# Kernel optimization log

Hardware: AMD Instinct MI355X
Metric: run time of the kernel (lower is better)

## Reference

```python
import jax, jax.numpy as jnp
import numpy as np

B, N, D = 8, 1024, 768
R, SH = 10, 2
H = R + SH            # 12 total heads
DH = D // H           # 64
DF = 2 * D            # FFN hidden


def _layernorm(x, g, b, eps=1e-5):
    mu = jnp.mean(x, axis=-1, keepdims=True)
    var = jnp.var(x, axis=-1, keepdims=True)
    return (x - mu) * jax.lax.rsqrt(var + eps) * g + b


def setup_inputs() -> dict:
    key = jax.random.key(0)
    ks = jax.random.split(key, 12)
    s = 0.02
    inp = {
        'nodes': jax.random.normal(ks[0], (B, N, D), dtype=jnp.float32),
        'relation_mask': jax.random.uniform(ks[1], (B, N, N, R), dtype=jnp.float32),
        'node_mask': jax.random.randint(ks[2], (B, N), 0, 2).astype(bool),
        'Wq': jax.random.normal(ks[3], (D, D), dtype=jnp.float32) * s,
        'bq': jnp.zeros((D,), jnp.float32),
        'Wk': jax.random.normal(ks[4], (D, D), dtype=jnp.float32) * s,
        'bk': jnp.zeros((D,), jnp.float32),
        'Wv': jax.random.normal(ks[5], (D, D), dtype=jnp.float32) * s,
        'bv': jnp.zeros((D,), jnp.float32),
        'Wo': jax.random.normal(ks[6], (D, D), dtype=jnp.float32) * s,
        'bo': jnp.zeros((D,), jnp.float32),
        'ln1_g': jnp.ones((D,), jnp.float32),
        'ln1_b': jnp.zeros((D,), jnp.float32),
        'W1': jax.random.normal(ks[7], (DF, D), dtype=jnp.float32) * s,
        'b1': jnp.zeros((DF,), jnp.float32),
        'W2': jax.random.normal(ks[8], (D, DF), dtype=jnp.float32) * s,
        'b2': jnp.zeros((D,), jnp.float32),
        'ln2_g': jnp.ones((D,), jnp.float32),
        'ln2_b': jnp.zeros((D,), jnp.float32),
    }
    return inp


def reference(nodes, relation_mask, node_mask, Wq, bq, Wk, bk, Wv, bv, Wo, bo,
              ln1_g, ln1_b, W1, b1, W2, b2, ln2_g, ln2_b):
    neg_inf = jnp.float32(-jnp.inf)
    # projections -> [B, H, N, DH]
    q = (nodes @ Wq.T + bq).reshape(B, N, H, DH).transpose(0, 2, 1, 3)
    k = (nodes @ Wk.T + bk).reshape(B, N, H, DH).transpose(0, 2, 1, 3)
    v = (nodes @ Wv.T + bv).reshape(B, N, H, DH).transpose(0, 2, 1, 3)
    scores = jnp.einsum('bhqd,bhkd->bhqk', q, k) / jnp.sqrt(jnp.float32(DH))
    # relation-typed gating on first R heads
    rel_gate = relation_mask.transpose(0, 3, 1, 2)          # [B, R, N, N]
    typed = jnp.where(rel_gate < 1e-4, neg_inf, scores[:, :R])
    scores = jnp.concatenate([typed, scores[:, R:]], axis=1)
    # key padding mask
    key_mask = node_mask[:, None, None, :]                  # [B,1,1,N]
    scores = jnp.where(key_mask, scores, neg_inf)
    attn = jax.nn.softmax(scores, axis=-1)
    attn = jnp.nan_to_num(attn, nan=0.0)                    # rows with no valid keys -> 0
    out = jnp.einsum('bhqk,bhkd->bhqd', attn, v)
    out = out.transpose(0, 2, 1, 3).reshape(B, N, D)
    out = out @ Wo.T + bo
    h = _layernorm(nodes + out, ln1_g, ln1_b)
    ffn = jax.nn.gelu(h @ W1.T + b1, approximate=False) @ W2.T + b2
    h = _layernorm(h + ffn, ln2_g, ln2_b)
    return h
```

## Files before the change

### kernel.cpp

```cpp
#include <hip/hip_runtime.h>
#include <stdint.h>
#include <math.h>

typedef unsigned short u16;
typedef __bf16 bf16x8 __attribute__((ext_vector_type(8)));
typedef unsigned short u16x8 __attribute__((ext_vector_type(8)));
typedef unsigned short us4 __attribute__((ext_vector_type(4)));
typedef float f32x4 __attribute__((ext_vector_type(4)));

#define DEVI __device__ __forceinline__

constexpr int B_ = 8, N_ = 1024, D_ = 768, H_ = 12, DH_ = 64, DF_ = 1536;

DEVI u16 f2bu(float f) {
  unsigned x = __builtin_bit_cast(unsigned, f);
  x += 0x7FFFu + ((x >> 16) & 1u);
  return (u16)(x >> 16);
}
DEVI float b2f(u16 u) { return __builtin_bit_cast(float, (unsigned)u << 16); }

DEVI bf16x8 ld_frag(const u16* p) {
  return __builtin_bit_cast(bf16x8, *(const u16x8*)p);
}

DEVI void gload_lds16(const u16* g, u16* l) {
  __builtin_amdgcn_global_load_lds(
      (const __attribute__((address_space(1))) void*)g,
      (__attribute__((address_space(3))) void*)l, 16, 0, 0);
}

struct CvtArgs {
  const float* src[7];
  u16* dst[7];
  int n4[7];
  int start[8];
};
__global__ __launch_bounds__(256)
void cvt_all(CvtArgs a) {
  const int gb = blockIdx.x;
  int j = 0;
  while (gb >= a.start[j + 1]) ++j;
  const int i = (gb - a.start[j]) * 256 + threadIdx.x;
  if (i >= a.n4[j]) return;
  float4 v = ((const float4*)a.src[j])[i];
  ushort4 o;
  o.x = f2bu(v.x); o.y = f2bu(v.y); o.z = f2bu(v.z); o.w = f2bu(v.w);
  ((ushort4*)a.dst[j])[i] = o;
}

__global__ __launch_bounds__(256)
void build_mask_packed(const float* __restrict__ rel, const int* __restrict__ nm,
                       u16* __restrict__ mp) {
  const int b = blockIdx.z, q0 = blockIdx.y * 16, k0 = blockIdx.x * 256;
  const int t = threadIdx.x;
  __shared__ u16 w12[16][256];
  const int key_ok = nm[(b << 10) + k0 + t];
  const float th = 1e-4f;
#pragma unroll 1
  for (int it = 0; it < 16; ++it) {
    unsigned bits;
    if (!key_ok) {
      bits = 0xFFFu;
    } else {
      const size_t idx = (((size_t)(b << 10) + q0 + it) << 10) + k0 + t;
      const float2* rp = (const float2*)(rel + idx * 10);
      float2 a0 = rp[0], a1 = rp[1], a2 = rp[2], a3 = rp[3], a4 = rp[4];
      bits  = (a0.x < th ? 1u : 0u)   | (a0.y < th ? 2u : 0u)
            | (a1.x < th ? 4u : 0u)   | (a1.y < th ? 8u : 0u)
            | (a2.x < th ? 16u : 0u)  | (a2.y < th ? 32u : 0u)
            | (a3.x < th ? 64u : 0u)  | (a3.y < th ? 128u : 0u)
            | (a4.x < th ? 256u : 0u) | (a4.y < th ? 512u : 0u);
    }
    w12[it][t ^ ((it & 7) << 1)] = (u16)bits;
  }
  __syncthreads();
  const int ql = t & 15, kt = t >> 4;
  unsigned wv[16];
#pragma unroll
  for (int j2 = 0; j2 < 8; ++j2) {
    const int e = (kt * 16 + j2 * 2) ^ ((ql & 7) << 1);
    wv[j2 * 2] = w12[ql][e];
    wv[j2 * 2 + 1] = w12[ql][e + 1];
  }
#pragma unroll
  for (int h = 0; h < 12; ++h) {
    unsigned word = 0;
#pragma unroll
    for (int j = 0; j < 16; ++j) word |= ((wv[j] >> h) & 1u) << j;
    mp[(((size_t)(b * H_ + h)) * (N_ / 16) + (k0 >> 4) + kt) * N_ + q0 + ql] = (u16)word;
  }
}

template<int EPI>
__global__ __launch_bounds__(256, 3)
void gemm_bt(const u16* __restrict__ A, const u16* __restrict__ Bm,
             const float* __restrict__ bias0, const float* __restrict__ bias1,
             const float* __restrict__ residf, const u16* __restrict__ residb,
             u16* __restrict__ out0, u16* __restrict__ out1,
             int M, int N, int K) {
  __shared__ u16 As[3][128 * 32];
  __shared__ u16 Bs[3][128 * 32];
  const int t = threadIdx.x;
  const int w = t >> 6, l = t & 63;
  const int li = l & 15, grp = l >> 4;
  const int nwg = gridDim.x * gridDim.y;
  int id = blockIdx.y * gridDim.x + blockIdx.x;
  id = (id & 7) * (nwg >> 3) + (id >> 3);
  const int by = id / gridDim.x;
  const int bx = id - by * gridDim.x;
  const int n0 = bx * 128, m0 = by * 128;
  const int wr = w >> 1, wc = w & 1;

  f32x4 acc[4][4] = {};

  const int arow = w * 16 + (l >> 2);
  const int acol = (l & 3) * 8;
  const u16* Ag = A + (size_t)(m0 + arow) * K + acol;
  const u16* Bg = Bm + (size_t)(n0 + arow) * K + acol;
  const int NT = K >> 5;

  auto stage = [&](int buf, int kt) {
    u16* Asw = &As[buf][(w * 16) * 32];
    u16* Bsw = &Bs[buf][(w * 16) * 32];
    const int k0 = kt * 32;
    gload_lds16(Ag + k0, Asw);
    gload_lds16(Ag + (size_t)64 * K + k0, Asw + 64 * 32);
    gload_lds16(Bg + k0, Bsw);
    gload_lds16(Bg + (size_t)64 * K + k0, Bsw + 64 * 32);
  };

  stage(0, 0); stage(1, 1);
  asm volatile("s_waitcnt vmcnt(4)\n\ts_barrier" ::: "memory");

  for (int kt = 0; kt < NT; ++kt) {
    const int bt = kt % 3;
    const bool pre = (kt + 2 < NT);
    if (pre) stage((kt + 2) % 3, kt + 2);
    bf16x8 af[4], bfr[4];
#pragma unroll
    for (int m = 0; m < 4; ++m)
      af[m] = ld_frag(&As[bt][(wr * 64 + m * 16 + li) * 32 + grp * 8]);
#pragma unroll
    for (int n = 0; n < 4; ++n)
      bfr[n] = ld_frag(&Bs[bt][(wc * 64 + n * 16 + li) * 32 + grp * 8]);
    __builtin_amdgcn_s_setprio(1);
#pragma unroll
    for (int m = 0; m < 4; ++m)
#pragma unroll
      for (int n = 0; n < 4; ++n)
        acc[m][n] = __builtin_amdgcn_mfma_f32_16x16x32_bf16(af[m], bfr[n], acc[m][n], 0, 0, 0);
    __builtin_amdgcn_s_setprio(0);
    if (pre) asm volatile("s_waitcnt vmcnt(4) lgkmcnt(0)\n\ts_barrier" ::: "memory");
    else     asm volatile("s_waitcnt vmcnt(0) lgkmcnt(0)\n\ts_barrier" ::: "memory");
  }

#pragma unroll
  for (int m = 0; m < 4; ++m) {
#pragma unroll
    for (int n = 0; n < 4; ++n) {
#pragma unroll
      for (int j = 0; j < 4; ++j) {
        const int row = m0 + wr * 64 + m * 16 + grp * 4 + j;
        const int col = n0 + wc * 64 + n * 16 + li;
        float v = acc[m][n][j];
        if constexpr (EPI == 0) {
          v += (col < D_) ? bias0[col] : bias1[col - D_];
          if (col < D_) v *= 0.125f;
          const int b = row >> 10, i = row & (N_ - 1);
          int c2 = (col < D_) ? col : col - D_;
          u16* dst = (col < D_) ? out0 : out1;
          dst[(((size_t)(b * H_ + (c2 >> 6))) * N_ + i) * DH_ + (c2 & 63)] = f2bu(v);
        } else if constexpr (EPI == 1) {
          v += bias0[row];
          const int b = col >> 10, i = col & (N_ - 1);
          out0[(((size_t)(b * H_ + (row >> 6))) * DH_ + (row & 63)) * N_ + i] = f2bu(v);
        } else if constexpr (EPI == 2) {
          v += bias0[col] + residf[(size_t)row * N + col];
          out0[(size_t)row * N + col] = f2bu(v);
        } else if constexpr (EPI == 3) {
          v += bias0[col];
          float gel = 0.5f * v * (1.0f + erff(v * 0.70710678118654752440f));
          out0[(size_t)row * N + col] = f2bu(gel);
        } else {
          v += bias0[col] + b2f(residb[(size_t)row * N + col]);
          out0[(size_t)row * N + col] = f2bu(v);
        }
      }
    }
  }
}

__global__ __launch_bounds__(512, 4)
void attn(const u16* __restrict__ q, const u16* __restrict__ k, const u16* __restrict__ vT,
          const u16* __restrict__ mp, u16* __restrict__ outp) {
  const int nwg = gridDim.x;
  const int p = blockIdx.x;
  const int lid = (p & 7) * (nwg >> 3) + (p >> 3);
  const int bh_i = lid >> 3;
  const int qblk = lid & 7;
  const int b = bh_i / H_, h = bh_i - (bh_i / H_) * H_;
  const int w = threadIdx.x >> 6, l = threadIdx.x & 63;
  const int li = l & 15, grp = l >> 4;
  const int qw = qblk * 128 + w * 16;
  const size_t bh = (size_t)bh_i;

  __shared__ u16 Kt[2][64 * 64];
  __shared__ u16 Vt[2][64 * 64];
  __shared__ u16 P[8][16 * 64];

  const u16* kbase = k + bh * N_ * DH_;
  const u16* vbase = vT + bh * DH_ * N_;

  const int srow_off = l >> 3;
  const int sg = l & 7;
  const int r0 = w * 8;
  auto stageK = [&](int buf, int kj0) {
    const int row = r0 + srow_off;
    const int gp = sg ^ (row & 7);
    gload_lds16(kbase + (size_t)(kj0 + row) * DH_ + gp * 8, &Kt[buf][r0 * 64]);
  };
  auto stageV = [&](int buf, int kj0) {
    const int row = r0 + srow_off;
    const int gp = sg ^ (row & 7);
    gload_lds16(vbase + (size_t)row * N_ + kj0 + gp * 8, &Vt[buf][r0 * 64]);
  };

  const u16* qp = q + (bh * N_ + qw) * DH_;
  const bf16x8 bq0 = ld_frag(qp + li * DH_ + grp * 8);
  const bf16x8 bq1 = ld_frag(qp + li * DH_ + 32 + grp * 8);

  f32x4 accO[4] = {};
  float m = -INFINITY, lsum = 0.f;

  u16* Pw = &P[w][0];
  const int sw = (li & 7) << 3;
  const int prow = li * 64;
  const u16* mrow = mp + bh * (N_ / 16) * N_ + qw + li;

  stageK(0, 0); stageV(0, 0);
  __syncthreads();
  int cur = 0;

  for (int kj0 = 0; kj0 < N_; kj0 += 64) {
    if (kj0 + 64 < N_) { stageK(cur ^ 1, kj0 + 64); stageV(cur ^ 1, kj0 + 64); }
    unsigned mword[4];
#pragma unroll
    for (int t = 0; t < 4; ++t) mword[t] = mrow[(size_t)((kj0 >> 4) + t) * N_];

    f32x4 s[4];
    __builtin_amdgcn_s_setprio(1);
#pragma unroll
    for (int t = 0; t < 4; ++t) {
      const int row = t * 16 + li;
      const int rs = row & 7;
      const bf16x8 ka0 = ld_frag(&Kt[cur][row * 64 + ((grp ^ rs) * 8)]);
      const bf16x8 ka1 = ld_frag(&Kt[cur][row * 64 + (((grp + 4) ^ rs) * 8)]);
      f32x4 z = {0.f, 0.f, 0.f, 0.f};
      z = __builtin_amdgcn_mfma_f32_16x16x32_bf16(ka0, bq0, z, 0, 0, 0);
      z = __builtin_amdgcn_mfma_f32_16x16x32_bf16(ka1, bq1, z, 0, 0, 0);
      s[t] = z;
    }
    __builtin_amdgcn_s_setprio(0);

    float sv[16];
    float rmax = -INFINITY;
#pragma unroll
    for (int t = 0; t < 4; ++t) {
      const unsigned mb = (mword[t] >> (grp * 4)) & 0xFu;
#pragma unroll
      for (int j = 0; j < 4; ++j) {
        const float x = ((mb >> j) & 1u) ? -INFINITY : s[t][j];
        sv[t * 4 + j] = x;
        rmax = fmaxf(rmax, x);
      }
    }
    rmax = fmaxf(rmax, __shfl_xor(rmax, 16));
    rmax = fmaxf(rmax, __shfl_xor(rmax, 32));
    if (!__all(rmax <= m + 8.f)) {
      const float mnew = fmaxf(m, rmax);
      const float scal = (m == -INFINITY) ? 0.f : __expf(m - mnew);
      lsum *= scal;
#pragma unroll
      for (int t2 = 0; t2 < 4; ++t2) accO[t2] *= scal;
      m = mnew;
    }
    const float msafe = (m == -INFINITY) ? 0.f : m;
    float psum = 0.f;
    float pv[16];
#pragma unroll
    for (int i = 0; i < 16; ++i) {
      const float e = __expf(sv[i] - msafe);
      pv[i] = e;
      psum += e;
    }
    psum += __shfl_xor(psum, 16);
    psum += __shfl_xor(psum, 32);
    lsum += psum;
#pragma unroll
    for (int t = 0; t < 4; ++t) {
      us4 pk;
      pk[0] = f2bu(pv[t * 4 + 0]); pk[1] = f2bu(pv[t * 4 + 1]);
      pk[2] = f2bu(pv[t * 4 + 2]); pk[3] = f2bu(pv[t * 4 + 3]);
      *(us4*)&Pw[prow + ((t * 16 + grp * 4) ^ sw)] = pk;
    }
    __builtin_amdgcn_s_setprio(1);
#pragma unroll
    for (int kc = 0; kc < 2; ++kc) {
      const bf16x8 pb = ld_frag(&Pw[prow + ((kc * 32 + grp * 8) ^ sw)]);
#pragma unroll
      for (int t2 = 0; t2 < 4; ++t2) {
        const int row = t2 * 16 + li;
        const bf16x8 va = ld_frag(&Vt[cur][row * 64 + (((kc * 4 + grp) ^ (row & 7)) * 8)]);
        accO[t2] = __builtin_amdgcn_mfma_f32_16x16x32_bf16(va, pb, accO[t2], 0, 0, 0);
      }
    }
    __builtin_amdgcn_s_setprio(0);
    __syncthreads();
    cur ^= 1;
  }
  const float inv = (lsum > 0.f) ? 1.0f / lsum : 0.f;
  u16* op = outp + ((size_t)b * N_ + qw + li) * D_ + h * DH_;
#pragma unroll
  for (int t2 = 0; t2 < 4; ++t2) {
    us4 ov;
    ov[0] = f2bu(accO[t2][0] * inv); ov[1] = f2bu(accO[t2][1] * inv);
    ov[2] = f2bu(accO[t2][2] * inv); ov[3] = f2bu(accO[t2][3] * inv);
    *(us4*)&op[t2 * 16 + grp * 4] = ov;
  }
}

template<int OUTF32>
__global__ __launch_bounds__(256)
void ln_kernel(const u16* __restrict__ x, const float* __restrict__ g,
               const float* __restrict__ be, u16* __restrict__ ybf,
               float* __restrict__ yf) {
  const int row = blockIdx.x;
  const int t = threadIdx.x;
  const u16* xr = x + (size_t)row * D_;
  const float v0 = b2f(xr[t]), v1 = b2f(xr[t + 256]), v2 = b2f(xr[t + 512]);
  float s = v0 + v1 + v2;
  float s2 = v0 * v0 + v1 * v1 + v2 * v2;
#pragma unroll
  for (int d = 1; d < 64; d <<= 1) { s += __shfl_xor(s, d); s2 += __shfl_xor(s2, d); }
  __shared__ float red[8];
  const int w = t >> 6;
  if ((t & 63) == 0) { red[w] = s; red[4 + w] = s2; }
  __syncthreads();
  s = red[0] + red[1] + red[2] + red[3];
  s2 = red[4] + red[5] + red[6] + red[7];
  const float mu = s * (1.0f / D_);
  const float var = fmaxf(s2 * (1.0f / D_) - mu * mu, 0.0f);
  const float rstd = rsqrtf(var + 1e-5f);
#pragma unroll
  for (int c = 0; c < 3; ++c) {
    const int idx = t + c * 256;
    const float vv = (c == 0) ? v0 : (c == 1) ? v1 : v2;
    const float o = (vv - mu) * rstd * g[idx] + be[idx];
    if constexpr (OUTF32) yf[(size_t)row * D_ + idx] = o;
    else ybf[(size_t)row * D_ + idx] = f2bu(o);
  }
}

extern "C" void kernel_launch(void* const* d_in, const int* in_sizes, int n_in,
                              void* d_out, int out_size, void* d_ws, size_t ws_size,
                              hipStream_t stream) {
  (void)in_sizes; (void)n_in; (void)out_size; (void)ws_size;
  const float* nodes = (const float*)d_in[0];
  const float* rel   = (const float*)d_in[1];
  const int*   nmask = (const int*)d_in[2];
  const float* Wq = (const float*)d_in[3];
  const float* bq = (const float*)d_in[4];
  const float* Wk = (const float*)d_in[5];
  const float* bk = (const float*)d_in[6];
  const float* Wv = (const float*)d_in[7];
  const float* bv = (const float*)d_in[8];
  const float* Wo = (const float*)d_in[9];
  const float* bo = (const float*)d_in[10];
  const float* ln1g = (const float*)d_in[11];
  const float* ln1b = (const float*)d_in[12];
  const float* W1 = (const float*)d_in[13];
  const float* b1 = (const float*)d_in[14];
  const float* W2 = (const float*)d_in[15];
  const float* b2 = (const float*)d_in[16];
  const float* ln2g = (const float*)d_in[17];
  const float* ln2b = (const float*)d_in[18];
  float* out = (float*)d_out;

  char* ws = (char*)d_ws;
  u16* Wqk_bf = (u16*)(ws + 0);
  u16* Wv_bf  = (u16*)(ws + 2359296);
  u16* Wo_bf  = (u16*)(ws + 3538944);
  u16* W1_bf  = (u16*)(ws + 4718592);
  u16* W2_bf  = (u16*)(ws + 7077888);
  u16* Xbf    = (u16*)(ws + 9437184);
  u16* qb     = (u16*)(ws + 22020096);
  u16* kb     = (u16*)(ws + 34603008);
  u16* vTb    = (u16*)(ws + 47185920);
  u16* mwb    = (u16*)(ws + 59768832);
  u16* prehb  = (u16*)(ws + 22020096);
  u16* hbf    = (u16*)(ws + 47185920);
  u16* f1b    = (u16*)(ws + 59768832);
  u16* preob  = (u16*)(ws + 84934656);
  u16* attno  = Xbf;

  const dim3 blk(256);
  build_mask_packed<<<dim3(4, 64, 8), blk, 0, stream>>>(rel, nmask, mwb);
  CvtArgs ca;
  ca.src[0] = Wq; ca.src[1] = Wk; ca.src[2] = Wv; ca.src[3] = Wo;
  ca.src[4] = W1; ca.src[5] = W2; ca.src[6] = nodes;
  ca.dst[0] = Wqk_bf; ca.dst[1] = Wqk_bf + 768 * 768; ca.dst[2] = Wv_bf;
  ca.dst[3] = Wo_bf; ca.dst[4] = W1_bf; ca.dst[5] = W2_bf; ca.dst[6] = Xbf;
  ca.n4[0] = ca.n4[1] = ca.n4[2] = ca.n4[3] = 147456;
  ca.n4[4] = ca.n4[5] = 294912; ca.n4[6] = 1572864;
  ca.start[0] = 0; ca.start[1] = 576; ca.start[2] = 1152; ca.start[3] = 1728;
  ca.start[4] = 2304; ca.start[5] = 3456; ca.start[6] = 4608; ca.start[7] = 10752;
  cvt_all<<<10752, blk, 0, stream>>>(ca);
  gemm_bt<0><<<dim3(12, 64), blk, 0, stream>>>(Xbf, Wqk_bf, bq, bk, nullptr, nullptr,
                                               qb, kb, 8192, 1536, 768);
  gemm_bt<1><<<dim3(64, 6), blk, 0, stream>>>(Wv_bf, Xbf, bv, nullptr, nullptr, nullptr,
                                              vTb, nullptr, 768, 8192, 768);
  attn<<<768, dim3(512), 0, stream>>>(qb, kb, vTb, mwb, attno);
  gemm_bt<2><<<dim3(6, 64), blk, 0, stream>>>(attno, Wo_bf, bo, nullptr, nodes, nullptr,
                                              prehb, nullptr, 8192, 768, 768);
  ln_kernel<0><<<8192, blk, 0, stream>>>(prehb, ln1g, ln1b, hbf, nullptr);
  gemm_bt<3><<<dim3(12, 64), blk, 0, stream>>>(hbf, W1_bf, b1, nullptr, nullptr, nullptr,
                                               f1b, nullptr, 8192, 1536, 768);
  gemm_bt<4><<<dim3(6, 64), blk, 0, stream>>>(f1b, W2_bf, b2, nullptr, nullptr, hbf,
                                              preob, nullptr, 8192, 768, 1536);
  ln_kernel<1><<<8192, blk, 0, stream>>>(preob, ln2g, ln2b, nullptr, out);
}
```

Before: 310.9 us.

## Merge mask build with conversion and fuse QK and V projection GEMMs into one launch

Folds the relation-mask packing kernel into the fp32-to-bf16 conversion kernel as extra leading blocks, and merges the Q/K projection GEMM with the transposed V projection GEMM into a single grid of 1152 tiles. This cuts two kernel launches and lets small grids share the device, which reduces tail idle time. The attention kernel also gets a tree-shaped row max and uses native bf16 conversion for packing P and the output. Risks: the mask blocks use shared memory and a barrier inside a branch, and native bf16 casts may round differently from the manual f2bu.

```diff
diff --git a/kernel.cpp b/kernel.cpp
--- a/kernel.cpp
+++ b/kernel.cpp
@@ -4,8 +4,8 @@
 
 typedef unsigned short u16;
 typedef __bf16 bf16x8 __attribute__((ext_vector_type(8)));
+typedef __bf16 bf16x2 __attribute__((ext_vector_type(2)));
 typedef unsigned short u16x8 __attribute__((ext_vector_type(8)));
-typedef unsigned short us4 __attribute__((ext_vector_type(4)));
 typedef float f32x4 __attribute__((ext_vector_type(4)));
 
 #define DEVI __device__ __forceinline__
@@ -36,78 +36,70 @@
   int start[8];
 };
 __global__ __launch_bounds__(256)
-void cvt_all(CvtArgs a) {
-  const int gb = blockIdx.x;
-  int j = 0;
-  while (gb >= a.start[j + 1]) ++j;
-  const int i = (gb - a.start[j]) * 256 + threadIdx.x;
-  if (i >= a.n4[j]) return;
-  float4 v = ((const float4*)a.src[j])[i];
-  ushort4 o;
-  o.x = f2bu(v.x); o.y = f2bu(v.y); o.z = f2bu(v.z); o.w = f2bu(v.w);
-  ((ushort4*)a.dst[j])[i] = o;
-}
-
-__global__ __launch_bounds__(256)
-void build_mask_packed(const float* __restrict__ rel, const int* __restrict__ nm,
-                       u16* __restrict__ mp) {
-  const int b = blockIdx.z, q0 = blockIdx.y * 16, k0 = blockIdx.x * 256;
+void prep_all(CvtArgs a, const float* __restrict__ rel, const int* __restrict__ nm,
+              u16* __restrict__ mp) {
+  const int gb0 = blockIdx.x;
   const int t = threadIdx.x;
-  __shared__ u16 w12[16][256];
-  const int key_ok = nm[(b << 10) + k0 + t];
-  const float th = 1e-4f;
+  if (gb0 < 2048) {
+    const int b = gb0 >> 8, q0 = ((gb0 >> 2) & 63) * 16, k0 = (gb0 & 3) * 256;
+    __shared__ u16 w12[16][256];
+    const int key_ok = nm[(b << 10) + k0 + t];
+    const float th = 1e-4f;
 #pragma unroll 1
-  for (int it = 0; it < 16; ++it) {
-    unsigned bits;
-    if (!key_ok) {
-      bits = 0xFFFu;
-    } else {
-      const size_t idx = (((size_t)(b << 10) + q0 + it) << 10) + k0 + t;
-      const float2* rp = (const float2*)(rel + idx * 10);
-      float2 a0 = rp[0], a1 = rp[1], a2 = rp[2], a3 = rp[3], a4 = rp[4];
-      bits  = (a0.x < th ? 1u : 0u)   | (a0.y < th ? 2u : 0u)
-            | (a1.x < th ? 4u : 0u)   | (a1.y < th ? 8u : 0u)
-            | (a2.x < th ? 16u : 0u)  | (a2.y < th ? 32u : 0u)
-            | (a3.x < th ? 64u : 0u)  | (a3.y < th ? 128u : 0u)
-            | (a4.x < th ? 256u : 0u) | (a4.y < th ? 512u : 0u);
-    }
-    w12[it][t ^ ((it & 7) << 1)] = (u16)bits;
-  }
-  __syncthreads();
-  const int ql = t & 15, kt = t >> 4;
-  unsigned wv[16];
-#pragma unroll
-  for (int j2 = 0; j2 < 8; ++j2) {
-    const int e = (kt * 16 + j2 * 2) ^ ((ql & 7) << 1);
-    wv[j2 * 2] = w12[ql][e];
-    wv[j2 * 2 + 1] = w12[ql][e + 1];
-  }
-#pragma unroll
-  for (int h = 0; h < 12; ++h) {
-    unsigned word = 0;
-#pragma unroll
-    for (int j = 0; j < 16; ++j) word |= ((wv[j] >> h) & 1u) << j;
-    mp[(((size_t)(b * H_ + h)) * (N_ / 16) + (k0 >> 4) + kt) * N_ + q0 + ql] = (u16)word;
+    for (int it = 0; it < 16; ++it) {
+      unsigned bits;
+      if (!key_ok) {
+        bits = 0xFFFu;
+      } else {
+        const size_t idx = (((size_t)(b << 10) + q0 + it) << 10) + k0 + t;
+        const float2* rp = (const float2*)(rel + idx * 10);
+        float2 a0 = rp[0], a1 = rp[1], a2 = rp[2], a3 = rp[3], a4 = rp[4];
+        bits  = (a0.x < th ? 1u : 0u)   | (a0.y < th ? 2u : 0u)
+              | (a1.x < th ? 4u : 0u)   | (a1.y < th ? 8u : 0u)
+              | (a2.x < th ? 16u : 0u)  | (a2.y < th ? 32u : 0u)
+              | (a3.x < th ? 64u : 0u)  | (a3.y < th ? 128u : 0u)
+              | (a4.x < th ? 256u : 0u) | (a4.y < th ? 512u : 0u);
+      }
+      w12[it][t ^ ((it & 7) << 1)] = (u16)bits;
+    }
+    __syncthreads();
+    const int ql = t & 15, kt = t >> 4;
+    unsigned wv[16];
+#pragma unroll
+    for (int j2 = 0; j2 < 8; ++j2) {
+      const int e = (kt * 16 + j2 * 2) ^ ((ql & 7) << 1);
+      wv[j2 * 2] = w12[ql][e];
+      wv[j2 * 2 + 1] = w12[ql][e + 1];
+    }
+#pragma unroll
+    for (int h = 0; h < 12; ++h) {
+      unsigned word = 0;
+#pragma unroll
+      for (int j = 0; j < 16; ++j) word |= ((wv[j] >> h) & 1u) << j;
+      mp[(((size_t)(b * H_ + h)) * (N_ / 16) + (k0 >> 4) + kt) * N_ + q0 + ql] = (u16)word;
+    }
+  } else {
+    int j = 0;
+    while (gb0 >= a.start[j + 1]) ++j;
+    const int i = (gb0 - a.start[j]) * 256 + t;
+    if (i >= a.n4[j]) return;
+    float4 v = ((const float4*)a.src[j])[i];
+    ushort4 o;
+    o.x = f2bu(v.x); o.y = f2bu(v.y); o.z = f2bu(v.z); o.w = f2bu(v.w);
+    ((ushort4*)a.dst[j])[i] = o;
   }
 }
 
 template<int EPI>
-__global__ __launch_bounds__(256, 3)
-void gemm_bt(const u16* __restrict__ A, const u16* __restrict__ Bm,
-             const float* __restrict__ bias0, const float* __restrict__ bias1,
-             const float* __restrict__ residf, const u16* __restrict__ residb,
-             u16* __restrict__ out0, u16* __restrict__ out1,
-             int M, int N, int K) {
-  __shared__ u16 As[3][128 * 32];
-  __shared__ u16 Bs[3][128 * 32];
+DEVI void gemm_body(const u16* __restrict__ A, const u16* __restrict__ Bm,
+                    const float* __restrict__ bias0, const float* __restrict__ bias1,
+                    const float* __restrict__ residf, const u16* __restrict__ residb,
+                    u16* __restrict__ out0, u16* __restrict__ out1,
+                    int N, int K, int bx, int by,
+                    u16 (&As)[3][128 * 32], u16 (&Bs)[3][128 * 32]) {
   const int t = threadIdx.x;
   const int w = t >> 6, l = t & 63;
   const int li = l & 15, grp = l >> 4;
-  const int nwg = gridDim.x * gridDim.y;
-  int id = blockIdx.y * gridDim.x + blockIdx.x;
-  id = (id & 7) * (nwg >> 3) + (id >> 3);
-  const int by = id / gridDim.x;
-  const int bx = id - by * gridDim.x;
   const int n0 = bx * 128, m0 = by * 128;
   const int wr = w >> 1, wc = w & 1;
 
@@ -190,6 +182,46 @@
   }
 }
 
+template<int EPI>
+__global__ __launch_bounds__(256, 3)
+void gemm_bt(const u16* __restrict__ A, const u16* __restrict__ Bm,
+             const float* __restrict__ bias0,
+             const float* __restrict__ residf, const u16* __restrict__ residb,
+             u16* __restrict__ out0, int N, int K) {
+  __shared__ u16 As[3][128 * 32];
+  __shared__ u16 Bs[3][128 * 32];
+  const int nwg = gridDim.x * gridDim.y;
+  int id = blockIdx.y * gridDim.x + blockIdx.x;
+  id = (id & 7) * (nwg >> 3) + (id >> 3);
+  const int by = id / gridDim.x;
+  const int bx = id - by * gridDim.x;
+  gemm_body<EPI>(A, Bm, bias0, nullptr, residf, residb, out0, nullptr,
+                 N, K, bx, by, As, Bs);
+}
+
+__global__ __launch_bounds__(256, 3)
+void gemm_qkv(const u16* __restrict__ Xbf, const u16* __restrict__ Wqk,
+              const u16* __restrict__ Wv,
+              const float* __restrict__ bq, const float* __restrict__ bk,
+              const float* __restrict__ bv,
+              u16* __restrict__ qb, u16* __restrict__ kb, u16* __restrict__ vTb) {
+  __shared__ u16 As[3][128 * 32];
+  __shared__ u16 Bs[3][128 * 32];
+  constexpr int nwg = 1152;
+  int id = blockIdx.x;
+  id = (id & 7) * (nwg >> 3) + (id >> 3);
+  if (id < 768) {
+    const int by = id / 12, bx = id - by * 12;
+    gemm_body<0>(Xbf, Wqk, bq, bk, nullptr, nullptr, qb, kb,
+                 1536, 768, bx, by, As, Bs);
+  } else {
+    const int v = id - 768;
+    const int by = v / 64, bx = v - by * 64;
+    gemm_body<1>(Wv, Xbf, bv, nullptr, nullptr, nullptr, vTb, nullptr,
+                 8192, 768, bx, by, As, Bs);
+  }
+}
+
 __global__ __launch_bounds__(512, 4)
 void attn(const u16* __restrict__ q, const u16* __restrict__ k, const u16* __restrict__ vT,
           const u16* __restrict__ mp, u16* __restrict__ outp) {
@@ -263,17 +295,19 @@
     __builtin_amdgcn_s_setprio(0);
 
     float sv[16];
-    float rmax = -INFINITY;
 #pragma unroll
     for (int t = 0; t < 4; ++t) {
       const unsigned mb = (mword[t] >> (grp * 4)) & 0xFu;
 #pragma unroll
-      for (int j = 0; j < 4; ++j) {
-        const float x = ((mb >> j) & 1u) ? -INFINITY : s[t][j];
-        sv[t * 4 + j] = x;
-        rmax = fmaxf(rmax, x);
-      }
-    }
+      for (int j = 0; j < 4; ++j)
+        sv[t * 4 + j] = ((mb >> j) & 1u) ? -INFINITY : s[t][j];
+    }
+    const float a0 = fmaxf(fmaxf(sv[0], sv[1]), sv[2]);
+    const float a1 = fmaxf(fmaxf(sv[3], sv[4]), sv[5]);
+    const float a2 = fmaxf(fmaxf(sv[6], sv[7]), sv[8]);
+    const float a3 = fmaxf(fmaxf(sv[9], sv[10]), sv[11]);
+    const float a4 = fmaxf(fmaxf(sv[12], sv[13]), sv[14]);
+    float rmax = fmaxf(fmaxf(fmaxf(a0, a1), fmaxf(a2, a3)), fmaxf(a4, sv[15]));
     rmax = fmaxf(rmax, __shfl_xor(rmax, 16));
     rmax = fmaxf(rmax, __shfl_xor(rmax, 32));
     if (!__all(rmax <= m + 8.f)) {
@@ -298,10 +332,12 @@
     lsum += psum;
 #pragma unroll
     for (int t = 0; t < 4; ++t) {
-      us4 pk;
-      pk[0] = f2bu(pv[t * 4 + 0]); pk[1] = f2bu(pv[t * 4 + 1]);
-      pk[2] = f2bu(pv[t * 4 + 2]); pk[3] = f2bu(pv[t * 4 + 3]);
-      *(us4*)&Pw[prow + ((t * 16 + grp * 4) ^ sw)] = pk;
+      bf16x2 plo = { (__bf16)pv[t * 4 + 0], (__bf16)pv[t * 4 + 1] };
+      bf16x2 phi = { (__bf16)pv[t * 4 + 2], (__bf16)pv[t * 4 + 3] };
+      uint2 pk;
+      pk.x = __builtin_bit_cast(unsigned, plo);
+      pk.y = __builtin_bit_cast(unsigned, phi);
+      *(uint2*)&Pw[prow + ((t * 16 + grp * 4) ^ sw)] = pk;
     }
     __builtin_amdgcn_s_setprio(1);
 #pragma unroll
@@ -322,10 +358,12 @@
   u16* op = outp + ((size_t)b * N_ + qw + li) * D_ + h * DH_;
 #pragma unroll
   for (int t2 = 0; t2 < 4; ++t2) {
-    us4 ov;
-    ov[0] = f2bu(accO[t2][0] * inv); ov[1] = f2bu(accO[t2][1] * inv);
-    ov[2] = f2bu(accO[t2][2] * inv); ov[3] = f2bu(accO[t2][3] * inv);
-    *(us4*)&op[t2 * 16 + grp * 4] = ov;
+    bf16x2 o01 = { (__bf16)(accO[t2][0] * inv), (__bf16)(accO[t2][1] * inv) };
+    bf16x2 o23 = { (__bf16)(accO[t2][2] * inv), (__bf16)(accO[t2][3] * inv) };
+    uint2 ov;
+    ov.x = __builtin_bit_cast(unsigned, o01);
+    ov.y = __builtin_bit_cast(unsigned, o23);
+    *(uint2*)&op[t2 * 16 + grp * 4] = ov;
   }
 }
 
@@ -404,7 +442,6 @@
   u16* attno  = Xbf;
 
   const dim3 blk(256);
-  build_mask_packed<<<dim3(4, 64, 8), blk, 0, stream>>>(rel, nmask, mwb);
   CvtArgs ca;
   ca.src[0] = Wq; ca.src[1] = Wk; ca.src[2] = Wv; ca.src[3] = Wo;
   ca.src[4] = W1; ca.src[5] = W2; ca.src[6] = nodes;
@@ -412,20 +449,17 @@
   ca.dst[3] = Wo_bf; ca.dst[4] = W1_bf; ca.dst[5] = W2_bf; ca.dst[6] = Xbf;
   ca.n4[0] = ca.n4[1] = ca.n4[2] = ca.n4[3] = 147456;
   ca.n4[4] = ca.n4[5] = 294912; ca.n4[6] = 1572864;
-  ca.start[0] = 0; ca.start[1] = 576; ca.start[2] = 1152; ca.start[3] = 1728;
-  ca.start[4] = 2304; ca.start[5] = 3456; ca.start[6] = 4608; ca.start[7] = 10752;
-  cvt_all<<<10752, blk, 0, stream>>>(ca);
-  gemm_bt<0><<<dim3(12, 64), blk, 0, stream>>>(Xbf, Wqk_bf, bq, bk, nullptr, nullptr,
-                                               qb, kb, 8192, 1536, 768);
-  gemm_bt<1><<<dim3(64, 6), blk, 0, stream>>>(Wv_bf, Xbf, bv, nullptr, nullptr, nullptr,
-                                              vTb, nullptr, 768, 8192, 768);
+  ca.start[0] = 2048; ca.start[1] = 2624; ca.start[2] = 3200; ca.start[3] = 3776;
+  ca.start[4] = 4352; ca.start[5] = 5504; ca.start[6] = 6656; ca.start[7] = 12800;
+  prep_all<<<12800, blk, 0, stream>>>(ca, rel, nmask, mwb);
+  gemm_qkv<<<1152, blk, 0, stream>>>(Xbf, Wqk_bf, Wv_bf, bq, bk, bv, qb, kb, vTb);
   attn<<<768, dim3(512), 0, stream>>>(qb, kb, vTb, mwb, attno);
-  gemm_bt<2><<<dim3(6, 64), blk, 0, stream>>>(attno, Wo_bf, bo, nullptr, nodes, nullptr,
-                                              prehb, nullptr, 8192, 768, 768);
+  gemm_bt<2><<<dim3(6, 64), blk, 0, stream>>>(attno, Wo_bf, bo, nodes, nullptr,
+                                              prehb, 768, 768);
   ln_kernel<0><<<8192, blk, 0, stream>>>(prehb, ln1g, ln1b, hbf, nullptr);
-  gemm_bt<3><<<dim3(12, 64), blk, 0, stream>>>(hbf, W1_bf, b1, nullptr, nullptr, nullptr,
-                                               f1b, nullptr, 8192, 1536, 768);
-  gemm_bt<4><<<dim3(6, 64), blk, 0, stream>>>(f1b, W2_bf, b2, nullptr, nullptr, hbf,
-                                              preob, nullptr, 8192, 768, 1536);
+  gemm_bt<3><<<dim3(12, 64), blk, 0, stream>>>(hbf, W1_bf, b1, nullptr, nullptr,
+                                               f1b, 1536, 768);
+  gemm_bt<4><<<dim3(6, 64), blk, 0, stream>>>(f1b, W2_bf, b2, nullptr, hbf,
+                                              preob, 768, 1536);
   ln_kernel<1><<<8192, blk, 0, stream>>>(preob, ln2g, ln2b, nullptr, out);
 }
```

Result: faster. 298.5 us (-4.0%).
